# Performance work log

Measured on AMD Instinct MI355X. Metric: run time of the kernel, lower is better.

The kernel has to match this reference:

```python
import jax, jax.numpy as jnp
import numpy as np
from jax import lax

MID = 64      # mid_size -> token seq len = MID*MID = 4096
DM = 64       # d_model = in_channels
DI = 128      # d_inner = expand * d_model
DS = 16       # d_state
DC = 4        # d_conv
DTR = 4       # dt_rank = ceil(DM/16)
EPS = 1e-5


def conv3x3(x, w):
    return lax.conv_general_dilated(x, w, (1, 1), ((1, 1), (1, 1)),
                                    dimension_numbers=('NCHW', 'OIHW', 'NCHW'))


def layernorm(x, w, b):
    mu = jnp.mean(x, -1, keepdims=True)
    var = jnp.mean((x - mu) ** 2, -1, keepdims=True)
    return (x - mu) * lax.rsqrt(var + EPS) * w + b


def bilinear(x, h, w):
    b, c = x.shape[:2]
    return jax.image.resize(x, (b, c, h, w), method='bilinear', antialias=False)


def mamba(tok, in_w, conv_w, conv_b, xproj_w, dt_w, dt_b, Alog, D, out_w):
    # tok: (b, L, DM)
    b, L, _ = tok.shape
    xz = tok @ in_w.T                                # (b, L, 2*DI)
    xc, z = jnp.split(xz, 2, axis=-1)
    # causal depthwise conv1d over sequence
    xcT = xc.transpose(0, 2, 1)                      # (b, DI, L)
    xconv = lax.conv_general_dilated(xcT, conv_w, (1,), ((DC - 1, 0),),
                                     dimension_numbers=('NCH', 'OIH', 'NCH'),
                                     feature_group_count=DI)
    xconv = xconv + conv_b[None, :, None]
    u = jax.nn.silu(xconv.transpose(0, 2, 1))        # (b, L, DI)
    x_dbl = u @ xproj_w.T                            # (b, L, DTR+2*DS)
    dt, B, C = jnp.split(x_dbl, [DTR, DTR + DS], axis=-1)
    dt = jax.nn.softplus(dt @ dt_w.T + dt_b)         # (b, L, DI)
    A = -jnp.exp(Alog)                               # (DI, DS)
    dA = jnp.exp(dt[..., None] * A)                  # (b, L, DI, DS)
    dBu = dt[..., None] * B[:, :, None, :] * u[..., None]

    def step(h, xs):
        a_t, bu_t = xs
        h = a_t * h + bu_t
        return h, h

    h0 = jnp.zeros((b, DI, DS), dt.dtype)
    _, hs = lax.scan(step, h0, (dA.transpose(1, 0, 2, 3), dBu.transpose(1, 0, 2, 3)))
    y = jnp.einsum('lbns,bls->bln', hs, C) + u * D   # (b, L, DI)
    y = y * jax.nn.silu(z)
    return y @ out_w.T                               # (b, L, DM)


def setup_inputs() -> dict:
    key = jax.random.key(0)
    ks = iter(jax.random.split(key, 32))
    s = 0.02
    d = {}
    d['x'] = jax.random.normal(next(ks), (4, 64, 128, 128), jnp.float32)
    for n, shp in [('cb_w1', (64, 64, 3, 3)), ('cb_w2', (64, 64, 3, 3)),
                   ('sm_w1', (64, 64, 3, 3)), ('sm_w2', (64, 64, 3, 3))]:
        d[n] = jax.random.normal(next(ks), shp, jnp.float32) * s
    d['ln1_w'] = jnp.ones((DM,), jnp.float32); d['ln1_b'] = jnp.zeros((DM,), jnp.float32)
    d['ln2_w'] = jnp.ones((DM,), jnp.float32); d['ln2_b'] = jnp.zeros((DM,), jnp.float32)
    for p in ['m1', 'm2']:
        d[p + '_in_w'] = jax.random.normal(next(ks), (2 * DI, DM), jnp.float32) * s
        d[p + '_conv_w'] = jax.random.normal(next(ks), (DI, 1, DC), jnp.float32) * s
        d[p + '_conv_b'] = jnp.zeros((DI,), jnp.float32)
        d[p + '_xproj_w'] = jax.random.normal(next(ks), (DTR + 2 * DS, DI), jnp.float32) * s
        d[p + '_dt_w'] = jax.random.normal(next(ks), (DI, DTR), jnp.float32) * s
        d[p + '_dt_b'] = jnp.full((DI,), -2.0, jnp.float32)
        d[p + '_Alog'] = jnp.broadcast_to(jnp.log(jnp.arange(1, DS + 1, dtype=jnp.float32)), (DI, DS)).copy()
        d[p + '_D'] = jnp.ones((DI,), jnp.float32)
        d[p + '_out_w'] = jax.random.normal(next(ks), (DM, DI), jnp.float32) * s
    return d


def reference(x, cb_w1, cb_w2, ln1_w, ln1_b, ln2_w, ln2_b,
              m1_in_w, m1_conv_w, m1_conv_b, m1_xproj_w, m1_dt_w, m1_dt_b, m1_Alog, m1_D, m1_out_w,
              m2_in_w, m2_conv_w, m2_conv_b, m2_xproj_w, m2_dt_w, m2_dt_b, m2_Alog, m2_D, m2_out_w,
              sm_w1, sm_w2):
    b, c, h, w = x.shape
    xr = conv3x3(jax.nn.relu(conv3x3(x, cb_w1)), cb_w2) + x
    x_small = xr if (h, w) == (MID, MID) else bilinear(xr, MID, MID)
    tokens = x_small.reshape(b, c, MID * MID).transpose(0, 2, 1)   # (b, L, c)
    main = mamba(layernorm(tokens, ln1_w, ln1_b),
                 m1_in_w, m1_conv_w, m1_conv_b, m1_xproj_w, m1_dt_w, m1_dt_b, m1_Alog, m1_D, m1_out_w)
    gate_feat = mamba(layernorm(tokens, ln2_w, ln2_b),
                      m2_in_w, m2_conv_w, m2_conv_b, m2_xproj_w, m2_dt_w, m2_dt_b, m2_Alog, m2_D, m2_out_w)
    gate = jax.nn.softmax(gate_feat, axis=1)                       # softmax over token dim
    tokens = tokens + gate * main
    feat = tokens.transpose(0, 2, 1).reshape(b, c, MID, MID)
    if (h, w) != (MID, MID):
        feat = bilinear(feat, h, w)
    return conv3x3(jax.nn.relu(conv3x3(feat, sm_w1)), sm_w2)
```

## Files before the change

### kernel.cpp

```cpp
#include <hip/hip_runtime.h>

typedef unsigned int u32;
typedef unsigned short u16;
typedef __attribute__((ext_vector_type(8))) short short8;
typedef __attribute__((ext_vector_type(4))) float f32x4;

__device__ __forceinline__ float sigmoidf_(float x){
  return 1.f / (1.f + __expf(-x));
}
__device__ __forceinline__ u16 f2bf(float f){
  union { float f; u32 i; } v; v.f = f;
  u32 r = v.i + 0x7fffu + ((v.i >> 16) & 1u);
  return (u16)(r >> 16);
}
__device__ __forceinline__ float bf2f(u32 u){
  union { float f; u32 i; } v; v.i = (u & 0xffffu) << 16; return v.f;
}

__global__ void k_wswz2b(const float* __restrict__ wA, u16* __restrict__ WHA, u16* __restrict__ WLA,
                         const float* __restrict__ wB, u16* __restrict__ WHB, u16* __restrict__ WLB,
                         u16* __restrict__ BPH, u16* __restrict__ BPL){
  int gidx = blockIdx.x * 256 + threadIdx.x;
  if (gidx < 73728){
    int sel = gidx >= 36864;
    int idx = gidx - sel * 36864;
    const float* w = sel ? wB : wA;
    u16* WH = sel ? WHB : WHA;
    u16* WL = sel ? WLB : WLA;
    int j    = idx & 7;
    int lane = (idx >> 3) & 63;
    int nt   = (idx >> 9) & 3;
    int kc   = (idx >> 11) & 1;
    int t    = idx >> 12;
    int ic = kc * 32 + ((lane >> 4) & 3) * 8 + j;
    int oc = nt * 16 + (lane & 15);
    float v = w[(oc * 64 + ic) * 9 + t];
    u16 h = f2bf(v);
    u16 l = f2bf(v - bf2f(h));
    WH[idx] = h; WL[idx] = l;
  } else {
    int i = gidx - 73728;
    if (i >= 2064) return;
    int b = i / 516, p = i - b * 516;
    int y, x;
    if (p < 130){ y = 0; x = p; }
    else if (p < 260){ y = 129; x = p - 130; }
    else if (p < 388){ y = p - 260 + 1; x = 0; }
    else { y = p - 388 + 1; x = 129; }
    size_t o = (((size_t)b * 130 + y) * 130 + x) * 64;
    uint4 z = make_uint4(0, 0, 0, 0);
#pragma unroll
    for (int q = 0; q < 8; q++){
      *(uint4*)(BPH + o + q * 8) = z;
      *(uint4*)(BPL + o + q * 8) = z;
    }
  }
}

__global__ __launch_bounds__(256) void k_prep(const float* __restrict__ src,
                                              u16* __restrict__ PH, u16* __restrict__ PL){
  __shared__ float ld[64 * 129];
  int yp = blockIdx.x;
  int b  = blockIdx.y;
  int ys = yp - 1;
  int tid = threadIdx.x;
  if ((u32)ys < 128u){
    for (int i = tid; i < 8192; i += 256){
      int c = i >> 7, x = i & 127;
      ld[c * 129 + x] = src[((size_t)(b * 64 + c) * 128 + ys) * 128 + x];
    }
  }
  __syncthreads();
  for (int i = tid; i < 130 * 64; i += 256){
    int xp = i >> 6, c = i & 63;
    float v = 0.f;
    if ((u32)ys < 128u && (u32)(xp - 1) < 128u) v = ld[c * 129 + (xp - 1)];
    u16 h = f2bf(v);
    u16 l = f2bf(v - bf2f(h));
    size_t o = (((size_t)b * 130 + yp) * 130 + xp) * 64 + c;
    PH[o] = h; PL[o] = l;
  }
}

__global__ __launch_bounds__(256) void k_prepup(const float* __restrict__ FEAT,
                                                u16* __restrict__ PH, u16* __restrict__ PL){
  __shared__ float ld0[64 * 65], ld1[64 * 65];
  int yp = blockIdx.x;
  int b  = blockIdx.y;
  int ys = yp - 1;
  int tid = threadIdx.x;
  float wy = 0.f;
  if ((u32)ys < 128u){
    float ay = 0.5f * ys - 0.25f;
    int fy = (int)floorf(ay); wy = ay - fy;
    int y0s = fy < 0 ? 0 : fy, y1s = fy + 1 > 63 ? 63 : fy + 1;
    for (int i = tid; i < 1024; i += 256){
      int c = i >> 4, x4 = (i & 15) * 4;
      float4 a0 = *(const float4*)&FEAT[((size_t)(b * 64 + c) * 64 + y0s) * 64 + x4];
      float4 a1 = *(const float4*)&FEAT[((size_t)(b * 64 + c) * 64 + y1s) * 64 + x4];
      ld0[c * 65 + x4 + 0] = a0.x; ld0[c * 65 + x4 + 1] = a0.y;
      ld0[c * 65 + x4 + 2] = a0.z; ld0[c * 65 + x4 + 3] = a0.w;
      ld1[c * 65 + x4 + 0] = a1.x; ld1[c * 65 + x4 + 1] = a1.y;
      ld1[c * 65 + x4 + 2] = a1.z; ld1[c * 65 + x4 + 3] = a1.w;
    }
  }
  __syncthreads();
  for (int i = tid; i < 130 * 64; i += 256){
    int xp = i >> 6, c = i & 63;
    float v = 0.f;
    int xs = xp - 1;
    if ((u32)ys < 128u && (u32)xs < 128u){
      float ax = 0.5f * xs - 0.25f;
      int fx = (int)floorf(ax); float wx = ax - fx;
      int x0s = fx < 0 ? 0 : fx, x1s = fx + 1 > 63 ? 63 : fx + 1;
      float v0 = (1.f - wx) * ld0[c * 65 + x0s] + wx * ld0[c * 65 + x1s];
      float v1 = (1.f - wx) * ld1[c * 65 + x0s] + wx * ld1[c * 65 + x1s];
      v = (1.f - wy) * v0 + wy * v1;
    }
    u16 h = f2bf(v);
    u16 l = f2bf(v - bf2f(h));
    size_t o = (((size_t)b * 130 + yp) * 130 + xp) * 64 + c;
    PH[o] = h; PL[o] = l;
  }
}

__global__ __launch_bounds__(256) void k_convm(
    const u16* __restrict__ PH, const u16* __restrict__ PL,
    const u16* __restrict__ WH, const u16* __restrict__ WL,
    const float* __restrict__ resid,
    u16* __restrict__ OBH, u16* __restrict__ OBL,
    float* __restrict__ OUTF, float* __restrict__ T, float* __restrict__ NT,
    int mode)
{
  __shared__ __align__(16) u32 smem[9024];
  u16* Ah_s = (u16*)smem;
  u16* Al_s = Ah_s + 5760;
  int tid = threadIdx.x;
  int lane = tid & 63, w = tid >> 6;
  int quad = lane >> 4, lcol = lane & 15;
  int b = blockIdx.z, y0 = blockIdx.y * 8, x0 = blockIdx.x * 16;

  f32x4 acc[2][4];
#pragma unroll
  for (int mt = 0; mt < 2; mt++)
#pragma unroll
    for (int nt = 0; nt < 4; nt++)
      acc[mt][nt] = (f32x4){0.f, 0.f, 0.f, 0.f};

  for (int kc = 0; kc < 2; kc++){
    __syncthreads();
    for (int i = tid; i < 720; i += 256){
      int q = i & 3;
      int rc = i >> 2;
      int r = rc / 18, c = rc - r * 18;
      size_t so = (((size_t)b * 130 + y0 + r) * 130 + (x0 + c)) * 64 + kc * 32 + q * 8;
      int de = (r * 18 + c) * 32 + q * 8;
      *(uint4*)(Ah_s + de) = *(const uint4*)(PH + so);
      *(uint4*)(Al_s + de) = *(const uint4*)(PL + so);
    }
    __syncthreads();
#pragma unroll
    for (int t = 0; t < 9; t++){
      int dy = t / 3, dx = t - dy * 3;
      short8 bh[4], bl[4];
#pragma unroll
      for (int nt = 0; nt < 4; nt++){
        int o = ((t * 2 + kc) * 4 + nt) * 512 + lane * 8;
        bh[nt] = *(const short8*)(WH + o);
        bl[nt] = *(const short8*)(WL + o);
      }
      short8 ah[2], al[2];
#pragma unroll
      for (int mt = 0; mt < 2; mt++){
        int e = ((w * 2 + mt + dy) * 18 + (lcol + dx)) * 32 + quad * 8;
        ah[mt] = *(const short8*)(Ah_s + e);
        al[mt] = *(const short8*)(Al_s + e);
      }
#pragma unroll
      for (int mt = 0; mt < 2; mt++)
#pragma unroll
        for (int nt = 0; nt < 4; nt++){
          acc[mt][nt] = __builtin_amdgcn_mfma_f32_16x16x32_bf16(ah[mt], bh[nt], acc[mt][nt], 0, 0, 0);
          acc[mt][nt] = __builtin_amdgcn_mfma_f32_16x16x32_bf16(ah[mt], bl[nt], acc[mt][nt], 0, 0, 0);
          acc[mt][nt] = __builtin_amdgcn_mfma_f32_16x16x32_bf16(al[mt], bh[nt], acc[mt][nt], 0, 0, 0);
        }
    }
  }

  __syncthreads();
  if (mode == 0){
    u32* epi = smem;
#pragma unroll
    for (int mt = 0; mt < 2; mt++){
      int row = w * 2 + mt;
#pragma unroll
      for (int nt = 0; nt < 4; nt++){
#pragma unroll
        for (int reg = 0; reg < 4; reg++){
          float v = fmaxf(acc[mt][nt][reg], 0.f);
          u32 h = f2bf(v);
          u32 l = f2bf(v - bf2f(h));
          int ccol = quad * 4 + reg;
          int oc = nt * 16 + lcol;
          epi[(row * 16 + ccol) * 66 + oc] = h | (l << 16);
        }
      }
    }
    __syncthreads();
    for (int i = tid; i < 8192; i += 256){
      int px = i >> 6, oc = i & 63;
      int row = px >> 4, ccol = px & 15;
      u32 pk = epi[px * 66 + oc];
      size_t o = (((size_t)b * 130 + y0 + row + 1) * 130 + (x0 + ccol + 1)) * 64 + oc;
      OBH[o] = (u16)pk;
      OBL[o] = (u16)(pk >> 16);
    }
  } else {
    float* epi = (float*)smem;
#pragma unroll
    for (int mt = 0; mt < 2; mt++){
      int row = w * 2 + mt;
#pragma unroll
      for (int nt = 0; nt < 4; nt++){
#pragma unroll
        for (int reg = 0; reg < 4; reg++){
          int px = row * 16 + quad * 4 + reg;
          int oc = nt * 16 + lcol;
          epi[oc * 131 + px] = acc[mt][nt][reg];
        }
      }
    }
    __syncthreads();
    if (mode == 1){
      for (int i = tid; i < 8192; i += 256){
        int oc = i >> 7, px = i & 127;
        int row = px >> 4, c = px & 15;
        size_t o = (((size_t)b * 64 + oc) * 128 + y0 + row) * 128 + x0 + c;
        float v = epi[oc * 131 + px];
        if (resid) v += resid[o];
        OUTF[o] = v;
      }
    } else {
      for (int i = tid; i < 8192; i += 256){
        int oc = i >> 7, px = i & 127;
        int row = px >> 4, c = px & 15;
        size_t o = (((size_t)b * 64 + oc) * 128 + y0 + row) * 128 + x0 + c;
        epi[oc * 131 + px] += resid[o];
      }
      __syncthreads();
      float* redS  = (float*)smem + 8384;
      float* redQ  = redS + 288;
      float* stats = redQ + 288;
      int token = tid & 31, cgrp = tid >> 5;
      int tr = token >> 3, tc = token & 7;
      float av[8]; float s = 0.f, q = 0.f;
      int p0 = (2 * tr) * 16 + 2 * tc;
#pragma unroll
      for (int j = 0; j < 8; j++){
        int c = cgrp * 8 + j;
        const float* ep = epi + c * 131;
        float v = 0.25f * (ep[p0] + ep[p0 + 1] + ep[p0 + 16] + ep[p0 + 17]);
        av[j] = v; s += v; q = fmaf(v, v, q);
      }
      redS[token * 9 + cgrp] = s;
      redQ[token * 9 + cgrp] = q;
      __syncthreads();
      if (tid < 32){
        float S = 0.f, Q = 0.f;
        for (int g = 0; g < 8; g++){ S += redS[tid * 9 + g]; Q += redQ[tid * 9 + g]; }
        float mu = S * (1.f / 64.f);
        float var = Q * (1.f / 64.f) - mu * mu;
        stats[tid * 2] = mu;
        stats[tid * 2 + 1] = rsqrtf(var + 1e-5f);
      }
      __syncthreads();
      float mu = stats[token * 2], inv = stats[token * 2 + 1];
      int l = (blockIdx.y * 4 + tr) * 64 + blockIdx.x * 8 + tc;
      size_t to = ((size_t)b * 4096 + l) * 64 + cgrp * 8;
#pragma unroll
      for (int j = 0; j < 8; j++){
        T[to + j] = av[j];
        NT[to + j] = (av[j] - mu) * inv;
      }
    }
  }
}

__global__ __launch_bounds__(256) void k_fold2(
    const float* __restrict__ Wa, const float* __restrict__ lnwa, const float* __restrict__ lnba,
    float* __restrict__ W2a, float* __restrict__ B2a,
    const float* __restrict__ Wb, const float* __restrict__ lnwb, const float* __restrict__ lnbb,
    float* __restrict__ W2b, float* __restrict__ B2b){
  int m = blockIdx.x;
  const float* W   = m ? Wb   : Wa;
  const float* lnw = m ? lnwb : lnwa;
  const float* lnb = m ? lnbb : lnba;
  float* W2 = m ? W2b : W2a;
  float* B2 = m ? B2b : B2a;
  __shared__ float gw[64], gb[64];
  int j = threadIdx.x;
  if (j < 64){ gw[j] = lnw[j]; gb[j] = lnb[j]; }
  __syncthreads();
  float bias = 0.f;
#pragma unroll
  for (int k4 = 0; k4 < 16; k4++){
    float4 wv = *(const float4*)&W[j * 64 + k4 * 4];
    W2[j * 64 + k4 * 4 + 0] = wv.x * gw[k4 * 4 + 0];
    W2[j * 64 + k4 * 4 + 1] = wv.y * gw[k4 * 4 + 1];
    W2[j * 64 + k4 * 4 + 2] = wv.z * gw[k4 * 4 + 2];
    W2[j * 64 + k4 * 4 + 3] = wv.w * gw[k4 * 4 + 3];
    bias = fmaf(wv.x, gb[k4 * 4 + 0], bias);
    bias = fmaf(wv.y, gb[k4 * 4 + 1], bias);
    bias = fmaf(wv.z, gb[k4 * 4 + 2], bias);
    bias = fmaf(wv.w, gb[k4 * 4 + 3], bias);
  }
  B2[j] = bias;
}

__global__ __launch_bounds__(256) void k_inprojdw(
    const float* __restrict__ NT,
    const float* __restrict__ W2a, const float* __restrict__ B2a,
    float* __restrict__ Ua, float* __restrict__ Za,
    const float* __restrict__ cwa, const float* __restrict__ cba,
    const float* __restrict__ W2b, const float* __restrict__ B2b,
    float* __restrict__ Ub, float* __restrict__ Zb,
    const float* __restrict__ cwb, const float* __restrict__ cbb)
{
  __shared__ float wL[64 * 68];
  __shared__ float xcs[67 * 68];
  int mz = blockIdx.z;
  const float* W2 = mz ? W2b : W2a;
  const float* B2 = mz ? B2b : B2a;
  float* U = mz ? Ub : Ua;
  float* Z  = mz ? Zb : Za;
  const float* cw = mz ? cwb : cwa;
  const float* cb = mz ? cbb : cba;
  int tid = threadIdx.x;
  int t0 = blockIdx.x * 64;
  int j0 = blockIdx.y * 64;
  for (int i = tid; i < 4096; i += 256){
    int jl = i >> 6, k = i & 63;
    wL[jl * 68 + k] = W2[(size_t)(j0 + jl) * 64 + k];
  }
  __syncthreads();
  int tq = tid >> 4, cg = tid & 15;
  const float* ntp = NT + (size_t)(t0 + tq * 4) * 64;
  float acc[4][4];
#pragma unroll
  for (int c = 0; c < 4; c++){
    float bias = B2[j0 + cg + c * 16];
#pragma unroll
    for (int t = 0; t < 4; t++) acc[t][c] = bias;
  }
#pragma unroll 4
  for (int k4 = 0; k4 < 16; k4++){
    float4 lv[4];
#pragma unroll
    for (int t = 0; t < 4; t++)
      lv[t] = *(const float4*)(ntp + t * 64 + k4 * 4);
    float4 wv[4];
#pragma unroll
    for (int c = 0; c < 4; c++)
      wv[c] = *(const float4*)&wL[(cg + c * 16) * 68 + k4 * 4];
#pragma unroll
    for (int t = 0; t < 4; t++)
#pragma unroll
      for (int c = 0; c < 4; c++){
        acc[t][c] = fmaf(lv[t].x, wv[c].x, acc[t][c]);
        acc[t][c] = fmaf(lv[t].y, wv[c].y, acc[t][c]);
        acc[t][c] = fmaf(lv[t].z, wv[c].z, acc[t][c]);
        acc[t][c] = fmaf(lv[t].w, wv[c].w, acc[t][c]);
      }
  }
  if (j0 < 128){
    int isStart = ((t0 & 4095) == 0);
    if (tid < 192){
      int e = tid >> 6, col = tid & 63;
      float v = 0.f;
      if (!isStart){
        const float* np = NT + (size_t)(t0 - 3 + e) * 64;
        float a2 = B2[j0 + col];
#pragma unroll 4
        for (int k = 0; k < 64; k += 4){
          float4 nv = *(const float4*)(np + k);
          float4 wv = *(const float4*)&wL[col * 68 + k];
          a2 = fmaf(nv.x, wv.x, fmaf(nv.y, wv.y, fmaf(nv.z, wv.z, fmaf(nv.w, wv.w, a2))));
        }
        v = a2;
      }
      xcs[e * 68 + col] = v;
    }
#pragma unroll
    for (int t = 0; t < 4; t++)
#pragma unroll
      for (int c = 0; c < 4; c++)
        xcs[(3 + tq * 4 + t) * 68 + cg + c * 16] = acc[t][c];
    __syncthreads();
#pragma unroll
    for (int c = 0; c < 4; c++){
      int lc = cg + c * 16;
      int ch = j0 + lc;
      float4 wv = *(const float4*)(cw + ch * 4);
      float bias = cb[ch];
#pragma unroll
      for (int t = 0; t < 4; t++){
        int row = 3 + tq * 4 + t;
        float a = bias;
        a = fmaf(wv.w, xcs[row * 68 + lc], a);
        a = fmaf(wv.z, xcs[(row - 1) * 68 + lc], a);
        a = fmaf(wv.y, xcs[(row - 2) * 68 + lc], a);
        a = fmaf(wv.x, xcs[(row - 3) * 68 + lc], a);
        size_t tg = t0 + tq * 4 + t;
        U[tg * 128 + ch] = a * sigmoidf_(a);
      }
    }
  } else {
#pragma unroll
    for (int t = 0; t < 4; t++){
      size_t tg = t0 + tq * 4 + t;
#pragma unroll
      for (int c = 0; c < 4; c++)
        Z[tg * 128 + (j0 - 128) + cg + c * 16] = acc[t][c];
    }
  }
}

__global__ __launch_bounds__(256) void k_xprojdt(
    const float* __restrict__ U0, const float* __restrict__ XW0,
    const float* __restrict__ DTW0, const float* __restrict__ DTB0,
    float* __restrict__ DBL0, float* __restrict__ DT0,
    const float* __restrict__ U1, const float* __restrict__ XW1,
    const float* __restrict__ DTW1, const float* __restrict__ DTB1,
    float* __restrict__ DBL1, float* __restrict__ DT1)
{
  __shared__ float xw[36 * 132];
  __shared__ float sdtr[128 * 4];
  int bid = blockIdx.x;
  int m = bid >> 7, blk = bid & 127;
  const float* Up   = m ? U1   : U0;
  const float* XWp  = m ? XW1  : XW0;
  const float* DTWp = m ? DTW1 : DTW0;
  const float* DTBp = m ? DTB1 : DTB0;
  float* DBLp = m ? DBL1 : DBL0;
  float* DTp  = m ? DT1  : DT0;
  int tid = threadIdx.x;
  for (int i = tid; i < 4608; i += 256)
    xw[(i >> 7) * 132 + (i & 127)] = XWp[i];
  __syncthreads();
  int slot = tid >> 2, jq = tid & 3;
  size_t tgA = (size_t)blk * 128 + slot;
  size_t tgB = tgA + 64;
  const float4* upA = (const float4*)(Up + tgA * 128);
  const float4* upB = (const float4*)(Up + tgB * 128);
  float accA[9], accB[9];
#pragma unroll
  for (int jj = 0; jj < 9; jj++){ accA[jj] = 0.f; accB[jj] = 0.f; }
  for (int k4 = 0; k4 < 32; k4++){
    float4 uA = upA[k4];
    float4 uB = upB[k4];
#pragma unroll
    for (int jj = 0; jj < 9; jj++){
      float4 w = *(const float4*)&xw[(jq * 9 + jj) * 132 + k4 * 4];
      accA[jj] = fmaf(w.x, uA.x, fmaf(w.y, uA.y, fmaf(w.z, uA.z, fmaf(w.w, uA.w, accA[jj]))));
      accB[jj] = fmaf(w.x, uB.x, fmaf(w.y, uB.y, fmaf(w.z, uB.z, fmaf(w.w, uB.w, accB[jj]))));
    }
  }
#pragma unroll
  for (int jj = 0; jj < 9; jj++){
    DBLp[tgA * 36 + jq * 9 + jj] = accA[jj];
    DBLp[tgB * 36 + jq * 9 + jj] = accB[jj];
  }
  if (jq == 0){
#pragma unroll
    for (int jj = 0; jj < 4; jj++){
      sdtr[slot * 4 + jj] = accA[jj];
      sdtr[(slot + 64) * 4 + jj] = accB[jj];
    }
  }
  __syncthreads();
  int ch = tid & 127, half = tid >> 7;
  float4 wv = *(const float4*)(DTWp + ch * 4);
  float bias = DTBp[ch];
  for (int i = 0; i < 64; i++){
    int tl = half * 64 + i;
    float4 d = *(const float4*)&sdtr[tl * 4];
    float x = bias;
    x = fmaf(wv.x, d.x, x); x = fmaf(wv.y, d.y, x);
    x = fmaf(wv.z, d.z, x); x = fmaf(wv.w, d.w, x);
    x = fmaxf(x, 0.f) + log1pf(__expf(-fabsf(x)));
    DTp[((size_t)blk * 128 + tl) * 128 + ch] = x;
  }
}

__global__ __launch_bounds__(256) void k_scanA(
    const float* __restrict__ DT0, const float* __restrict__ DBL0, const float* __restrict__ U0,
    const float* __restrict__ AL0,
    const float* __restrict__ DT1, const float* __restrict__ DBL1, const float* __restrict__ U1,
    const float* __restrict__ AL1,
    float* __restrict__ HF, float* __restrict__ AP)
{
  __shared__ float sdt[64 * 65], su[64 * 65], sB[16 * 68];
  int bid = blockIdx.x;
  int cg = bid & 1;
  int c  = (bid >> 1) & 63;
  int b  = (bid >> 7) & 3;
  int m  = bid >> 9;
  const float* DTp  = m ? DT1  : DT0;
  const float* DBLp = m ? DBL1 : DBL0;
  const float* Up   = m ? U1   : U0;
  const float* ALp  = m ? AL1  : AL0;
  int tid = threadIdx.x;
  int lane = tid & 63, w = tid >> 6;
  int lcol = lane & 15, q = lane >> 4;
  int chL = w * 16 + lcol;
  int n = cg * 64 + chL;
  size_t base = (size_t)b * 4096 + c * 64;
  for (int i = tid; i < 4096; i += 256){
    int ch = i & 63, l = i >> 6;
    size_t off = (base + l) * 128 + cg * 64 + ch;
    sdt[l * 65 + ch] = DTp[off];
    su[l * 65 + ch]  = Up[off];
  }
  for (int i = tid; i < 1024; i += 256){
    int s = i & 15, l = i >> 4;
    sB[s * 68 + l] = DBLp[(base + l) * 36 + 4 + s];
  }
  float A1[4];
#pragma unroll
  for (int j = 0; j < 4; j++) A1[j] = -__expf(ALp[n * 16 + q * 4 + j]);
  __syncthreads();
  float h[4] = {0.f, 0.f, 0.f, 0.f};
  float ap[4] = {1.f, 1.f, 1.f, 1.f};
#pragma unroll
  for (int l4 = 0; l4 < 16; l4++){
    float4 Bv[4];
#pragma unroll
    for (int j = 0; j < 4; j++) Bv[j] = *(const float4*)&sB[(q * 4 + j) * 68 + l4 * 4];
#pragma unroll
    for (int jj = 0; jj < 4; jj++){
      int l = l4 * 4 + jj;
      float dt = sdt[l * 65 + chL];
      float u  = su[l * 65 + chL];
      float dtu = dt * u;
#pragma unroll
      for (int j = 0; j < 4; j++){
        float a = __expf(dt * A1[j]);
        h[j] = fmaf(a, h[j], dtu * (&Bv[j].x)[jj]);
        ap[j] *= a;
      }
    }
  }
  size_t o = ((size_t)((m * 4 + b) * 64 + c)) * 2048 + n * 16 + q * 4;
  *(float4*)&HF[o] = make_float4(h[0], h[1], h[2], h[3]);
  *(float4*)&AP[o] = make_float4(ap[0], ap[1], ap[2], ap[3]);
}

__global__ __launch_bounds__(64) void k_scanB(
    const float* __restrict__ HF, const float* __restrict__ AP, float* __restrict__ HIN)
{
  int r = blockIdx.x * 64 + threadIdx.x;
  int q = r >> 11;
  int p = r & 2047;
  float h = 0.f;
  for (int c = 0; c < 64; c++){
    size_t o = (size_t)(q * 64 + c) * 2048 + p;
    HIN[o] = h;
    h = fmaf(AP[o], h, HF[o]);
  }
}

__global__ __launch_bounds__(256) void k_scanC(
    const float* __restrict__ DT0, const float* __restrict__ DBL0, const float* __restrict__ U0,
    const float* __restrict__ AL0, const float* __restrict__ D0, float* __restrict__ Y0,
    const float* __restrict__ DT1, const float* __restrict__ DBL1, const float* __restrict__ U1,
    const float* __restrict__ AL1, const float* __restrict__ D1, float* __restrict__ Y1,
    const float* __restrict__ HIN)
{
  __shared__ float sdt[64 * 65], su[64 * 65], sB[16 * 68], sC[16 * 68];
  int bid = blockIdx.x;
  int cg = bid & 1;
  int c  = (bid >> 1) & 63;
  int b  = (bid >> 7) & 3;
  int m  = bid >> 9;
  const float* DTp  = m ? DT1  : DT0;
  const float* DBLp = m ? DBL1 : DBL0;
  const float* Up   = m ? U1   : U0;
  const float* ALp  = m ? AL1  : AL0;
  const float* Dp   = m ? D1   : D0;
  float*       Yp   = m ? Y1   : Y0;
  int tid = threadIdx.x;
  int lane = tid & 63, w = tid >> 6;
  int lcol = lane & 15, q = lane >> 4;
  int chL = w * 16 + lcol;
  int n = cg * 64 + chL;
  size_t base = (size_t)b * 4096 + c * 64;
  for (int i = tid; i < 4096; i += 256){
    int ch = i & 63, l = i >> 6;
    size_t off = (base + l) * 128 + cg * 64 + ch;
    sdt[l * 65 + ch] = DTp[off];
    su[l * 65 + ch]  = Up[off];
  }
  for (int i = tid; i < 1024; i += 256){
    int s = i & 15, l = i >> 4;
    size_t ob = (base + l) * 36;
    sB[s * 68 + l] = DBLp[ob + 4 + s];
    sC[s * 68 + l] = DBLp[ob + 20 + s];
  }
  float A1[4];
#pragma unroll
  for (int j = 0; j < 4; j++) A1[j] = -__expf(ALp[n * 16 + q * 4 + j]);
  float Dn = Dp[n];
  float4 hv = *(const float4*)&HIN[((size_t)((m * 4 + b) * 64 + c)) * 2048 + n * 16 + q * 4];
  float h[4] = {hv.x, hv.y, hv.z, hv.w};
  __syncthreads();
#pragma unroll
  for (int l4 = 0; l4 < 16; l4++){
    float4 Bv[4], Cv[4];
#pragma unroll
    for (int j = 0; j < 4; j++){
      Bv[j] = *(const float4*)&sB[(q * 4 + j) * 68 + l4 * 4];
      Cv[j] = *(const float4*)&sC[(q * 4 + j) * 68 + l4 * 4];
    }
#pragma unroll
    for (int jj = 0; jj < 4; jj++){
      int l = l4 * 4 + jj;
      float dt = sdt[l * 65 + chL];
      float u  = su[l * 65 + chL];
      float dtu = dt * u;
      float p = 0.f;
#pragma unroll
      for (int j = 0; j < 4; j++){
        float a = __expf(dt * A1[j]);
        h[j] = fmaf(a, h[j], dtu * (&Bv[j].x)[jj]);
        p = fmaf(h[j], (&Cv[j].x)[jj], p);
      }
      p += __shfl_xor(p, 16);
      p += __shfl_xor(p, 32);
      if (q == 0)
        Yp[(base + l) * 128 + n] = fmaf(u, Dn, p);
    }
  }
}

__global__ __launch_bounds__(256) void k_outproj(
    const float* __restrict__ Y0, const float* __restrict__ Zg0,
    const float* __restrict__ W0, float* __restrict__ OUT0,
    const float* __restrict__ Y1, const float* __restrict__ Zg1,
    const float* __restrict__ W1, float* __restrict__ OUT1)
{
  __shared__ float yl[16 * 128];
  __shared__ float wT[128 * 65];
  int m = blockIdx.y;
  const float* Y  = m ? Y1  : Y0;
  const float* Zg = m ? Zg1 : Zg0;
  const float* W  = m ? W1  : W0;
  float* OUT = m ? OUT1 : OUT0;
  int tid = threadIdx.x;
  size_t t0 = (size_t)blockIdx.x * 16;
  for (int i = tid; i < 2048; i += 256){
    float z = Zg[t0 * 128 + i];
    yl[i] = Y[t0 * 128 + i] * (z * sigmoidf_(z));
  }
  for (int i = tid; i < 8192; i += 256){
    int k = i & 127, j = i >> 7;
    wT[k * 65 + j] = W[j * 128 + k];
  }
  __syncthreads();
  int j = tid & 63;
  int tg = tid >> 6;
  float acc[4] = {0.f, 0.f, 0.f, 0.f};
  for (int k = 0; k < 128; k += 4){
    float w0 = wT[k * 65 + j], w1 = wT[(k+1) * 65 + j];
    float w2 = wT[(k+2) * 65 + j], w3 = wT[(k+3) * 65 + j];
#pragma unroll
    for (int t = 0; t < 4; t++){
      float4 yv = *(const float4*)&yl[(tg * 4 + t) * 128 + k];
      acc[t] = fmaf(w0, yv.x, fmaf(w1, yv.y, fmaf(w2, yv.z, fmaf(w3, yv.w, acc[t]))));
    }
  }
#pragma unroll
  for (int t = 0; t < 4; t++)
    OUT[(t0 + tg * 4 + t) * 64 + j] = acc[t];
}

__global__ void k_smA(const float* __restrict__ G, float* __restrict__ P){
  int bid = blockIdx.x;
  int b = bid >> 6, lc = bid & 63;
  int tid = threadIdx.x;
  int j = tid & 63, part = tid >> 6;
  size_t base = (size_t)b * 4096 + lc * 64;
  float mx = -3.4e38f;
  for (int i = 0; i < 16; i++){
    int l = part + i * 4;
    mx = fmaxf(mx, G[(base + l) * 64 + j]);
  }
  float sm = 0.f;
  for (int i = 0; i < 16; i++){
    int l = part + i * 4;
    sm += __expf(G[(base + l) * 64 + j] - mx);
  }
  __shared__ float sM[256], sS[256];
  sM[tid] = mx; sS[tid] = sm;
  __syncthreads();
  if (tid < 64){
    float M = sM[tid], S = sS[tid];
    for (int p = 1; p < 4; p++){
      float m2 = sM[p * 64 + tid], s2 = sS[p * 64 + tid];
      float Mn = fmaxf(M, m2);
      S = S * __expf(M - Mn) + s2 * __expf(m2 - Mn);
      M = Mn;
    }
    P[(bid * 64 + tid) * 2] = M;
    P[(bid * 64 + tid) * 2 + 1] = S;
  }
}

__global__ void k_smB(const float* __restrict__ P, float* __restrict__ F){
  int tid = threadIdx.x;
  int b = tid >> 6, j = tid & 63;
  float M = -3.4e38f, S = 0.f;
  for (int lc = 0; lc < 64; lc++){
    int idx = ((b * 64 + lc) * 64 + j) * 2;
    float m2 = P[idx], s2 = P[idx + 1];
    float Mn = fmaxf(M, m2);
    S = S * __expf(M - Mn) + s2 * __expf(m2 - Mn);
    M = Mn;
  }
  F[(b * 64 + j) * 2] = M;
  F[(b * 64 + j) * 2 + 1] = S;
}

__global__ void k_combine(const float* __restrict__ T, const float* __restrict__ MAIN,
                          const float* __restrict__ G, const float* __restrict__ F,
                          float* __restrict__ FEAT){
  int bid = blockIdx.x;
  int b = bid >> 6, row = bid & 63;
  int tid = threadIdx.x;
  int j = tid & 63, ls = tid >> 6;
  __shared__ float tile[64 * 65];
  float M = F[(b * 64 + j) * 2], invS = 1.f / F[(b * 64 + j) * 2 + 1];
  size_t lbase = (size_t)b * 4096 + row * 64;
  for (int i = 0; i < 16; i++){
    int col = ls + i * 4;
    size_t off = (lbase + col) * 64 + j;
    float g = __expf(G[off] - M) * invS;
    tile[col * 65 + j] = T[off] + g * MAIN[off];
  }
  __syncthreads();
  int colw = tid & 63, jr = tid >> 6;
  for (int jj = jr; jj < 64; jj += 4)
    FEAT[(((size_t)b * 64 + jj) * 64 + row) * 64 + colw] = tile[colw * 65 + jj];
}

extern "C" void kernel_launch(void* const* d_in, const int* in_sizes, int n_in,
                              void* d_out, int out_size, void* d_ws, size_t ws_size,
                              hipStream_t stream) {
  const size_t P1A = 0, P1B = 4326400;
  const size_t MB0 = 0, MB1 = 10027008;
  const size_t O_LN = 0, O_XC = 1048576, O_Z = 3145728, O_U = 5242880,
               O_DT = 7340032, O_DBL = 9437184;
  const size_t TOK = 20054016, OUT0 = 21102592, OUT1 = 22151168;
  const size_t FEAT = 23208448;
  const size_t P3A = 4194304, P3B = 8520704;
  const size_t WA_H = 19000000, WA_L = 19018432, WB_H = 19036864, WB_L = 19055296;
  const size_t PADN = 2163200;
  const size_t SMP = 0, SMF = 65536;
  const size_t W2_0 = 21102592, B2_0 = 21118976, W2_1 = 21119232, B2_1 = 21135616;
  const size_t TOTAL = 24257024;
  if (ws_size < TOTAL * 4) return;

  float* ws = (float*)d_ws;
  const float* X   = (const float*)d_in[0];
  const float* CB1 = (const float*)d_in[1];
  const float* CB2 = (const float*)d_in[2];
  const float* SW1 = (const float*)d_in[3];
  const float* SW2 = (const float*)d_in[4];
  const float* LNW[2] = { (const float*)d_in[5], (const float*)d_in[7] };
  const float* LNB[2] = { (const float*)d_in[6], (const float*)d_in[8] };
  const float *INW[2], *CW[2], *CBb[2], *XPW[2], *DTW[2], *DTB[2], *AL[2], *DD[2], *OW[2];
  for (int m = 0; m < 2; m++){
    int p = 9 + m * 9;
    INW[m] = (const float*)d_in[p + 0];
    CW[m]  = (const float*)d_in[p + 1];
    CBb[m] = (const float*)d_in[p + 2];
    XPW[m] = (const float*)d_in[p + 3];
    DTW[m] = (const float*)d_in[p + 4];
    DTB[m] = (const float*)d_in[p + 5];
    AL[m]  = (const float*)d_in[p + 6];
    DD[m]  = (const float*)d_in[p + 7];
    OW[m]  = (const float*)d_in[p + 8];
  }

  u16* wah = (u16*)(ws + WA_H); u16* wal = (u16*)(ws + WA_L);
  u16* wbh = (u16*)(ws + WB_H); u16* wbl = (u16*)(ws + WB_L);

  {
    u16* pah = (u16*)(ws + P1A); u16* pal = pah + PADN * 2;
    u16* pbh = (u16*)(ws + P1B); u16* pbl = pbh + PADN * 2;
    k_wswz2b<<<297, 256, 0, stream>>>(CB1, wah, wal, CB2, wbh, wbl, pbh, pbl);
    k_prep<<<dim3(130, 4), 256, 0, stream>>>(X, pah, pal);
    k_convm<<<dim3(8, 16, 4), 256, 0, stream>>>(pah, pal, wah, wal, nullptr,
                                                pbh, pbl, nullptr, nullptr, nullptr, 0);
    k_convm<<<dim3(8, 16, 4), 256, 0, stream>>>(pbh, pbl, wbh, wbl, X,
                                                nullptr, nullptr, nullptr,
                                                ws + TOK, ws + MB0 + O_LN, 2);
  }

  k_fold2<<<2, 256, 0, stream>>>(INW[0], LNW[0], LNB[0], ws + W2_0, ws + B2_0,
                                 INW[1], LNW[1], LNB[1], ws + W2_1, ws + B2_1);
  k_inprojdw<<<dim3(256, 4, 2), 256, 0, stream>>>(
      ws + MB0 + O_LN,
      ws + W2_0, ws + B2_0, ws + MB0 + O_U, ws + MB0 + O_Z, CW[0], CBb[0],
      ws + W2_1, ws + B2_1, ws + MB1 + O_U, ws + MB1 + O_Z, CW[1], CBb[1]);
  k_xprojdt<<<256, 256, 0, stream>>>(
      ws + MB0 + O_U, XPW[0], DTW[0], DTB[0], ws + MB0 + O_DBL, ws + MB0 + O_DT,
      ws + MB1 + O_U, XPW[1], DTW[1], DTB[1], ws + MB1 + O_DBL, ws + MB1 + O_DT);

  float* HF  = ws + MB0 + O_XC;
  float* AP  = ws + MB0 + O_XC + 1048576;
  float* HIN = ws + MB0 + O_LN;

  k_scanA<<<1024, 256, 0, stream>>>(
      ws + MB0 + O_DT, ws + MB0 + O_DBL, ws + MB0 + O_U, AL[0],
      ws + MB1 + O_DT, ws + MB1 + O_DBL, ws + MB1 + O_U, AL[1],
      HF, AP);
  k_scanB<<<256, 64, 0, stream>>>(HF, AP, HIN);
  k_scanC<<<1024, 256, 0, stream>>>(
      ws + MB0 + O_DT, ws + MB0 + O_DBL, ws + MB0 + O_U, AL[0], DD[0], ws + MB0 + O_XC,
      ws + MB1 + O_DT, ws + MB1 + O_DBL, ws + MB1 + O_U, AL[1], DD[1], ws + MB1 + O_XC,
      HIN);

  k_outproj<<<dim3(1024, 2), 256, 0, stream>>>(
      ws + MB0 + O_XC, ws + MB0 + O_Z, OW[0], ws + OUT0,
      ws + MB1 + O_XC, ws + MB1 + O_Z, OW[1], ws + OUT1);

  k_smA<<<256, 256, 0, stream>>>(ws + OUT1, ws + SMP);
  k_smB<<<1, 256, 0, stream>>>(ws + SMP, ws + SMF);
  k_combine<<<256, 256, 0, stream>>>(ws + TOK, ws + OUT0, ws + OUT1, ws + SMF, ws + FEAT);

  {
    u16* pah = (u16*)(ws + P3A); u16* pal = pah + PADN * 2;
    u16* pbh = (u16*)(ws + P3B); u16* pbl = pbh + PADN * 2;
    k_wswz2b<<<297, 256, 0, stream>>>(SW1, wah, wal, SW2, wbh, wbl, pbh, pbl);
    k_prepup<<<dim3(130, 4), 256, 0, stream>>>(ws + FEAT, pah, pal);
    k_convm<<<dim3(8, 16, 4), 256, 0, stream>>>(pah, pal, wah, wal, nullptr,
                                                pbh, pbl, nullptr, nullptr, nullptr, 0);
    k_convm<<<dim3(8, 16, 4), 256, 0, stream>>>(pbh, pbl, wbh, wbl, nullptr,
                                                nullptr, nullptr, (float*)d_out,
                                                nullptr, nullptr, 1);
  }
}
```

Before: 393.6 us.

## Enlarge conv tiles, recompute dt inside scan kernels, batch scanB loads

The conv kernel tile grows from 8x16 to 16x16 pixels per block, with 4 M-tiles per wave. This halves the grid and raises shared memory use, trading occupancy for more weight reuse and less halo overhead. The dt projection and softplus move out of k_xprojdt into both scan kernels, removing the large DT tensor's write and two reads at the cost of recomputing it twice. scanB now loads 8 steps of AP/HF before its serial recurrence to expose memory-level parallelism.

```diff
diff --git a/kernel.cpp b/kernel.cpp
--- a/kernel.cpp
+++ b/kernel.cpp
@@ -132,29 +132,29 @@
     float* __restrict__ OUTF, float* __restrict__ T, float* __restrict__ NT,
     int mode)
 {
-  __shared__ __align__(16) u32 smem[9024];
+  __shared__ __align__(16) u32 smem[17344];
   u16* Ah_s = (u16*)smem;
-  u16* Al_s = Ah_s + 5760;
+  u16* Al_s = Ah_s + 10368;
   int tid = threadIdx.x;
   int lane = tid & 63, w = tid >> 6;
   int quad = lane >> 4, lcol = lane & 15;
-  int b = blockIdx.z, y0 = blockIdx.y * 8, x0 = blockIdx.x * 16;
-
-  f32x4 acc[2][4];
-#pragma unroll
-  for (int mt = 0; mt < 2; mt++)
+  int b = blockIdx.z, y0 = blockIdx.y * 16, x0 = blockIdx.x * 16;
+
+  f32x4 acc[4][4];
+#pragma unroll
+  for (int mt = 0; mt < 4; mt++)
 #pragma unroll
     for (int nt = 0; nt < 4; nt++)
       acc[mt][nt] = (f32x4){0.f, 0.f, 0.f, 0.f};
 
   for (int kc = 0; kc < 2; kc++){
     __syncthreads();
-    for (int i = tid; i < 720; i += 256){
+    for (int i = tid; i < 1296; i += 256){
       int q = i & 3;
       int rc = i >> 2;
       int r = rc / 18, c = rc - r * 18;
       size_t so = (((size_t)b * 130 + y0 + r) * 130 + (x0 + c)) * 64 + kc * 32 + q * 8;
-      int de = (r * 18 + c) * 32 + q * 8;
+      int de = rc * 32 + q * 8;
       *(uint4*)(Ah_s + de) = *(const uint4*)(PH + so);
       *(uint4*)(Al_s + de) = *(const uint4*)(PL + so);
     }
@@ -169,15 +169,15 @@
         bh[nt] = *(const short8*)(WH + o);
         bl[nt] = *(const short8*)(WL + o);
       }
-      short8 ah[2], al[2];
-#pragma unroll
-      for (int mt = 0; mt < 2; mt++){
-        int e = ((w * 2 + mt + dy) * 18 + (lcol + dx)) * 32 + quad * 8;
+      short8 ah[4], al[4];
+#pragma unroll
+      for (int mt = 0; mt < 4; mt++){
+        int e = ((w * 4 + mt + dy) * 18 + (lcol + dx)) * 32 + quad * 8;
         ah[mt] = *(const short8*)(Ah_s + e);
         al[mt] = *(const short8*)(Al_s + e);
       }
 #pragma unroll
-      for (int mt = 0; mt < 2; mt++)
+      for (int mt = 0; mt < 4; mt++)
 #pragma unroll
         for (int nt = 0; nt < 4; nt++){
           acc[mt][nt] = __builtin_amdgcn_mfma_f32_16x16x32_bf16(ah[mt], bh[nt], acc[mt][nt], 0, 0, 0);
@@ -191,8 +191,8 @@
   if (mode == 0){
     u32* epi = smem;
 #pragma unroll
-    for (int mt = 0; mt < 2; mt++){
-      int row = w * 2 + mt;
+    for (int mt = 0; mt < 4; mt++){
+      int row = w * 4 + mt;
 #pragma unroll
       for (int nt = 0; nt < 4; nt++){
 #pragma unroll
@@ -207,7 +207,7 @@
       }
     }
     __syncthreads();
-    for (int i = tid; i < 8192; i += 256){
+    for (int i = tid; i < 16384; i += 256){
       int px = i >> 6, oc = i & 63;
       int row = px >> 4, ccol = px & 15;
       u32 pk = epi[px * 66 + oc];
@@ -218,56 +218,56 @@
   } else {
     float* epi = (float*)smem;
 #pragma unroll
-    for (int mt = 0; mt < 2; mt++){
-      int row = w * 2 + mt;
+    for (int mt = 0; mt < 4; mt++){
+      int row = w * 4 + mt;
 #pragma unroll
       for (int nt = 0; nt < 4; nt++){
 #pragma unroll
         for (int reg = 0; reg < 4; reg++){
           int px = row * 16 + quad * 4 + reg;
           int oc = nt * 16 + lcol;
-          epi[oc * 131 + px] = acc[mt][nt][reg];
+          epi[oc * 259 + px] = acc[mt][nt][reg];
         }
       }
     }
     __syncthreads();
     if (mode == 1){
-      for (int i = tid; i < 8192; i += 256){
-        int oc = i >> 7, px = i & 127;
+      for (int i = tid; i < 16384; i += 256){
+        int oc = i >> 8, px = i & 255;
         int row = px >> 4, c = px & 15;
         size_t o = (((size_t)b * 64 + oc) * 128 + y0 + row) * 128 + x0 + c;
-        float v = epi[oc * 131 + px];
+        float v = epi[oc * 259 + px];
         if (resid) v += resid[o];
         OUTF[o] = v;
       }
     } else {
-      for (int i = tid; i < 8192; i += 256){
-        int oc = i >> 7, px = i & 127;
+      for (int i = tid; i < 16384; i += 256){
+        int oc = i >> 8, px = i & 255;
         int row = px >> 4, c = px & 15;
         size_t o = (((size_t)b * 64 + oc) * 128 + y0 + row) * 128 + x0 + c;
-        epi[oc * 131 + px] += resid[o];
+        epi[oc * 259 + px] += resid[o];
       }
       __syncthreads();
-      float* redS  = (float*)smem + 8384;
-      float* redQ  = redS + 288;
-      float* stats = redQ + 288;
-      int token = tid & 31, cgrp = tid >> 5;
+      float* redS  = (float*)smem + 16576;
+      float* redQ  = redS + 320;
+      float* stats = redQ + 320;
+      int token = tid & 63, cg2 = tid >> 6;
       int tr = token >> 3, tc = token & 7;
-      float av[8]; float s = 0.f, q = 0.f;
+      float av[16]; float s = 0.f, q = 0.f;
       int p0 = (2 * tr) * 16 + 2 * tc;
 #pragma unroll
-      for (int j = 0; j < 8; j++){
-        int c = cgrp * 8 + j;
-        const float* ep = epi + c * 131;
+      for (int j = 0; j < 16; j++){
+        int c = cg2 * 16 + ((j + tr) & 15);
+        const float* ep = epi + c * 259;
         float v = 0.25f * (ep[p0] + ep[p0 + 1] + ep[p0 + 16] + ep[p0 + 17]);
         av[j] = v; s += v; q = fmaf(v, v, q);
       }
-      redS[token * 9 + cgrp] = s;
-      redQ[token * 9 + cgrp] = q;
+      redS[token * 5 + cg2] = s;
+      redQ[token * 5 + cg2] = q;
       __syncthreads();
-      if (tid < 32){
+      if (tid < 64){
         float S = 0.f, Q = 0.f;
-        for (int g = 0; g < 8; g++){ S += redS[tid * 9 + g]; Q += redQ[tid * 9 + g]; }
+        for (int g = 0; g < 4; g++){ S += redS[tid * 5 + g]; Q += redQ[tid * 5 + g]; }
         float mu = S * (1.f / 64.f);
         float var = Q * (1.f / 64.f) - mu * mu;
         stats[tid * 2] = mu;
@@ -275,12 +275,13 @@
       }
       __syncthreads();
       float mu = stats[token * 2], inv = stats[token * 2 + 1];
-      int l = (blockIdx.y * 4 + tr) * 64 + blockIdx.x * 8 + tc;
-      size_t to = ((size_t)b * 4096 + l) * 64 + cgrp * 8;
-#pragma unroll
-      for (int j = 0; j < 8; j++){
-        T[to + j] = av[j];
-        NT[to + j] = (av[j] - mu) * inv;
+      int l = (blockIdx.y * 8 + tr) * 64 + blockIdx.x * 8 + tc;
+      size_t to = ((size_t)b * 4096 + l) * 64;
+#pragma unroll
+      for (int j = 0; j < 16; j++){
+        int c = cg2 * 16 + ((j + tr) & 15);
+        T[to + c] = av[j];
+        NT[to + c] = (av[j] - mu) * inv;
       }
     }
   }
@@ -426,23 +427,15 @@
 }
 
 __global__ __launch_bounds__(256) void k_xprojdt(
-    const float* __restrict__ U0, const float* __restrict__ XW0,
-    const float* __restrict__ DTW0, const float* __restrict__ DTB0,
-    float* __restrict__ DBL0, float* __restrict__ DT0,
-    const float* __restrict__ U1, const float* __restrict__ XW1,
-    const float* __restrict__ DTW1, const float* __restrict__ DTB1,
-    float* __restrict__ DBL1, float* __restrict__ DT1)
+    const float* __restrict__ U0, const float* __restrict__ XW0, float* __restrict__ DBL0,
+    const float* __restrict__ U1, const float* __restrict__ XW1, float* __restrict__ DBL1)
 {
   __shared__ float xw[36 * 132];
-  __shared__ float sdtr[128 * 4];
   int bid = blockIdx.x;
   int m = bid >> 7, blk = bid & 127;
   const float* Up   = m ? U1   : U0;
   const float* XWp  = m ? XW1  : XW0;
-  const float* DTWp = m ? DTW1 : DTW0;
-  const float* DTBp = m ? DTB1 : DTB0;
   float* DBLp = m ? DBL1 : DBL0;
-  float* DTp  = m ? DT1  : DT0;
   int tid = threadIdx.x;
   for (int i = tid; i < 4608; i += 256)
     xw[(i >> 7) * 132 + (i & 127)] = XWp[i];
@@ -470,45 +463,26 @@
     DBLp[tgA * 36 + jq * 9 + jj] = accA[jj];
     DBLp[tgB * 36 + jq * 9 + jj] = accB[jj];
   }
-  if (jq == 0){
-#pragma unroll
-    for (int jj = 0; jj < 4; jj++){
-      sdtr[slot * 4 + jj] = accA[jj];
-      sdtr[(slot + 64) * 4 + jj] = accB[jj];
-    }
-  }
-  __syncthreads();
-  int ch = tid & 127, half = tid >> 7;
-  float4 wv = *(const float4*)(DTWp + ch * 4);
-  float bias = DTBp[ch];
-  for (int i = 0; i < 64; i++){
-    int tl = half * 64 + i;
-    float4 d = *(const float4*)&sdtr[tl * 4];
-    float x = bias;
-    x = fmaf(wv.x, d.x, x); x = fmaf(wv.y, d.y, x);
-    x = fmaf(wv.z, d.z, x); x = fmaf(wv.w, d.w, x);
-    x = fmaxf(x, 0.f) + log1pf(__expf(-fabsf(x)));
-    DTp[((size_t)blk * 128 + tl) * 128 + ch] = x;
-  }
 }
 
 __global__ __launch_bounds__(256) void k_scanA(
-    const float* __restrict__ DT0, const float* __restrict__ DBL0, const float* __restrict__ U0,
-    const float* __restrict__ AL0,
-    const float* __restrict__ DT1, const float* __restrict__ DBL1, const float* __restrict__ U1,
-    const float* __restrict__ AL1,
+    const float* __restrict__ DBL0, const float* __restrict__ U0, const float* __restrict__ AL0,
+    const float* __restrict__ DTW0, const float* __restrict__ DTB0,
+    const float* __restrict__ DBL1, const float* __restrict__ U1, const float* __restrict__ AL1,
+    const float* __restrict__ DTW1, const float* __restrict__ DTB1,
     float* __restrict__ HF, float* __restrict__ AP)
 {
-  __shared__ float sdt[64 * 65], su[64 * 65], sB[16 * 68];
+  __shared__ float sdt[64 * 65], su[64 * 65], sB[16 * 68], sdtr[256];
   int bid = blockIdx.x;
   int cg = bid & 1;
   int c  = (bid >> 1) & 63;
   int b  = (bid >> 7) & 3;
   int m  = bid >> 9;
-  const float* DTp  = m ? DT1  : DT0;
   const float* DBLp = m ? DBL1 : DBL0;
   const float* Up   = m ? U1   : U0;
   const float* ALp  = m ? AL1  : AL0;
+  const float* DTWp = m ? DTW1 : DTW0;
+  const float* DTBp = m ? DTB1 : DTB0;
   int tid = threadIdx.x;
   int lane = tid & 63, w = tid >> 6;
   int lcol = lane & 15, q = lane >> 4;
@@ -517,13 +491,31 @@
   size_t base = (size_t)b * 4096 + c * 64;
   for (int i = tid; i < 4096; i += 256){
     int ch = i & 63, l = i >> 6;
-    size_t off = (base + l) * 128 + cg * 64 + ch;
-    sdt[l * 65 + ch] = DTp[off];
-    su[l * 65 + ch]  = Up[off];
+    su[l * 65 + ch] = Up[(base + l) * 128 + cg * 64 + ch];
   }
   for (int i = tid; i < 1024; i += 256){
     int s = i & 15, l = i >> 4;
     sB[s * 68 + l] = DBLp[(base + l) * 36 + 4 + s];
+  }
+  if (tid < 256){
+    int l = tid >> 2, jj = tid & 3;
+    sdtr[tid] = DBLp[(base + l) * 36 + jj];
+  }
+  __syncthreads();
+  {
+    int chF = tid & 63;
+    float4 wdt = *(const float4*)(DTWp + (cg * 64 + chF) * 4);
+    float bdt = DTBp[cg * 64 + chF];
+#pragma unroll
+    for (int k = 0; k < 16; k++){
+      int l = (tid >> 6) + k * 4;
+      float4 d = *(const float4*)&sdtr[l * 4];
+      float x = bdt;
+      x = fmaf(wdt.x, d.x, x); x = fmaf(wdt.y, d.y, x);
+      x = fmaf(wdt.z, d.z, x); x = fmaf(wdt.w, d.w, x);
+      x = fmaxf(x, 0.f) + log1pf(__expf(-fabsf(x)));
+      sdt[l * 65 + chF] = x;
+    }
   }
   float A1[4];
 #pragma unroll
@@ -561,31 +553,44 @@
   int r = blockIdx.x * 64 + threadIdx.x;
   int q = r >> 11;
   int p = r & 2047;
+  size_t base = (size_t)q * 64 * 2048 + p;
   float h = 0.f;
-  for (int c = 0; c < 64; c++){
-    size_t o = (size_t)(q * 64 + c) * 2048 + p;
-    HIN[o] = h;
-    h = fmaf(AP[o], h, HF[o]);
+  for (int c8 = 0; c8 < 8; c8++){
+    float a[8], f[8];
+#pragma unroll
+    for (int j = 0; j < 8; j++){
+      size_t o = base + (size_t)(c8 * 8 + j) * 2048;
+      a[j] = AP[o]; f[j] = HF[o];
+    }
+#pragma unroll
+    for (int j = 0; j < 8; j++){
+      size_t o = base + (size_t)(c8 * 8 + j) * 2048;
+      HIN[o] = h;
+      h = fmaf(a[j], h, f[j]);
+    }
   }
 }
 
 __global__ __launch_bounds__(256) void k_scanC(
-    const float* __restrict__ DT0, const float* __restrict__ DBL0, const float* __restrict__ U0,
-    const float* __restrict__ AL0, const float* __restrict__ D0, float* __restrict__ Y0,
-    const float* __restrict__ DT1, const float* __restrict__ DBL1, const float* __restrict__ U1,
-    const float* __restrict__ AL1, const float* __restrict__ D1, float* __restrict__ Y1,
+    const float* __restrict__ DBL0, const float* __restrict__ U0, const float* __restrict__ AL0,
+    const float* __restrict__ DTW0, const float* __restrict__ DTB0,
+    const float* __restrict__ D0, float* __restrict__ Y0,
+    const float* __restrict__ DBL1, const float* __restrict__ U1, const float* __restrict__ AL1,
+    const float* __restrict__ DTW1, const float* __restrict__ DTB1,
+    const float* __restrict__ D1, float* __restrict__ Y1,
     const float* __restrict__ HIN)
 {
-  __shared__ float sdt[64 * 65], su[64 * 65], sB[16 * 68], sC[16 * 68];
+  __shared__ float sdt[64 * 65], su[64 * 65], sB[16 * 68], sC[16 * 68], sdtr[256];
   int bid = blockIdx.x;
   int cg = bid & 1;
   int c  = (bid >> 1) & 63;
   int b  = (bid >> 7) & 3;
   int m  = bid >> 9;
-  const float* DTp  = m ? DT1  : DT0;
   const float* DBLp = m ? DBL1 : DBL0;
   const float* Up   = m ? U1   : U0;
   const float* ALp  = m ? AL1  : AL0;
+  const float* DTWp = m ? DTW1 : DTW0;
+  const float* DTBp = m ? DTB1 : DTB0;
   const float* Dp   = m ? D1   : D0;
   float*       Yp   = m ? Y1   : Y0;
   int tid = threadIdx.x;
@@ -596,15 +601,33 @@
   size_t base = (size_t)b * 4096 + c * 64;
   for (int i = tid; i < 4096; i += 256){
     int ch = i & 63, l = i >> 6;
-    size_t off = (base + l) * 128 + cg * 64 + ch;
-    sdt[l * 65 + ch] = DTp[off];
-    su[l * 65 + ch]  = Up[off];
+    su[l * 65 + ch] = Up[(base + l) * 128 + cg * 64 + ch];
   }
   for (int i = tid; i < 1024; i += 256){
     int s = i & 15, l = i >> 4;
     size_t ob = (base + l) * 36;
     sB[s * 68 + l] = DBLp[ob + 4 + s];
     sC[s * 68 + l] = DBLp[ob + 20 + s];
+  }
+  if (tid < 256){
+    int l = tid >> 2, jj = tid & 3;
+    sdtr[tid] = DBLp[(base + l) * 36 + jj];
+  }
+  __syncthreads();
+  {
+    int chF = tid & 63;
+    float4 wdt = *(const float4*)(DTWp + (cg * 64 + chF) * 4);
+    float bdt = DTBp[cg * 64 + chF];
+#pragma unroll
+    for (int k = 0; k < 16; k++){
+      int l = (tid >> 6) + k * 4;
+      float4 d = *(const float4*)&sdtr[l * 4];
+      float x = bdt;
+      x = fmaf(wdt.x, d.x, x); x = fmaf(wdt.y, d.y, x);
+      x = fmaf(wdt.z, d.z, x); x = fmaf(wdt.w, d.w, x);
+      x = fmaxf(x, 0.f) + log1pf(__expf(-fabsf(x)));
+      sdt[l * 65 + chF] = x;
+    }
   }
   float A1[4];
 #pragma unroll
@@ -758,7 +781,7 @@
   const size_t P1A = 0, P1B = 4326400;
   const size_t MB0 = 0, MB1 = 10027008;
   const size_t O_LN = 0, O_XC = 1048576, O_Z = 3145728, O_U = 5242880,
-               O_DT = 7340032, O_DBL = 9437184;
+               O_DBL = 9437184;
   const size_t TOK = 20054016, OUT0 = 21102592, OUT1 = 22151168;
   const size_t FEAT = 23208448;
   const size_t P3A = 4194304, P3B = 8520704;
@@ -799,11 +822,11 @@
     u16* pbh = (u16*)(ws + P1B); u16* pbl = pbh + PADN * 2;
     k_wswz2b<<<297, 256, 0, stream>>>(CB1, wah, wal, CB2, wbh, wbl, pbh, pbl);
     k_prep<<<dim3(130, 4), 256, 0, stream>>>(X, pah, pal);
-    k_convm<<<dim3(8, 16, 4), 256, 0, stream>>>(pah, pal, wah, wal, nullptr,
-                                                pbh, pbl, nullptr, nullptr, nullptr, 0);
-    k_convm<<<dim3(8, 16, 4), 256, 0, stream>>>(pbh, pbl, wbh, wbl, X,
-                                                nullptr, nullptr, nullptr,
-                                                ws + TOK, ws + MB0 + O_LN, 2);
+    k_convm<<<dim3(8, 8, 4), 256, 0, stream>>>(pah, pal, wah, wal, nullptr,
+                                               pbh, pbl, nullptr, nullptr, nullptr, 0);
+    k_convm<<<dim3(8, 8, 4), 256, 0, stream>>>(pbh, pbl, wbh, wbl, X,
+                                               nullptr, nullptr, nullptr,
+                                               ws + TOK, ws + MB0 + O_LN, 2);
   }
 
   k_fold2<<<2, 256, 0, stream>>>(INW[0], LNW[0], LNB[0], ws + W2_0, ws + B2_0,
@@ -813,21 +836,21 @@
       ws + W2_0, ws + B2_0, ws + MB0 + O_U, ws + MB0 + O_Z, CW[0], CBb[0],
       ws + W2_1, ws + B2_1, ws + MB1 + O_U, ws + MB1 + O_Z, CW[1], CBb[1]);
   k_xprojdt<<<256, 256, 0, stream>>>(
-      ws + MB0 + O_U, XPW[0], DTW[0], DTB[0], ws + MB0 + O_DBL, ws + MB0 + O_DT,
-      ws + MB1 + O_U, XPW[1], DTW[1], DTB[1], ws + MB1 + O_DBL, ws + MB1 + O_DT);
+      ws + MB0 + O_U, XPW[0], ws + MB0 + O_DBL,
+      ws + MB1 + O_U, XPW[1], ws + MB1 + O_DBL);
 
   float* HF  = ws + MB0 + O_XC;
   float* AP  = ws + MB0 + O_XC + 1048576;
   float* HIN = ws + MB0 + O_LN;
 
   k_scanA<<<1024, 256, 0, stream>>>(
-      ws + MB0 + O_DT, ws + MB0 + O_DBL, ws + MB0 + O_U, AL[0],
-      ws + MB1 + O_DT, ws + MB1 + O_DBL, ws + MB1 + O_U, AL[1],
+      ws + MB0 + O_DBL, ws + MB0 + O_U, AL[0], DTW[0], DTB[0],
+      ws + MB1 + O_DBL, ws + MB1 + O_U, AL[1], DTW[1], DTB[1],
       HF, AP);
   k_scanB<<<256, 64, 0, stream>>>(HF, AP, HIN);
   k_scanC<<<1024, 256, 0, stream>>>(
-      ws + MB0 + O_DT, ws + MB0 + O_DBL, ws + MB0 + O_U, AL[0], DD[0], ws + MB0 + O_XC,
-      ws + MB1 + O_DT, ws + MB1 + O_DBL, ws + MB1 + O_U, AL[1], DD[1], ws + MB1 + O_XC,
+      ws + MB0 + O_DBL, ws + MB0 + O_U, AL[0], DTW[0], DTB[0], DD[0], ws + MB0 + O_XC,
+      ws + MB1 + O_DBL, ws + MB1 + O_U, AL[1], DTW[1], DTB[1], DD[1], ws + MB1 + O_XC,
       HIN);
 
   k_outproj<<<dim3(1024, 2), 256, 0, stream>>>(
@@ -843,10 +866,10 @@
     u16* pbh = (u16*)(ws + P3B); u16* pbl = pbh + PADN * 2;
     k_wswz2b<<<297, 256, 0, stream>>>(SW1, wah, wal, SW2, wbh, wbl, pbh, pbl);
     k_prepup<<<dim3(130, 4), 256, 0, stream>>>(ws + FEAT, pah, pal);
-    k_convm<<<dim3(8, 16, 4), 256, 0, stream>>>(pah, pal, wah, wal, nullptr,
-                                                pbh, pbl, nullptr, nullptr, nullptr, 0);
-    k_convm<<<dim3(8, 16, 4), 256, 0, stream>>>(pbh, pbl, wbh, wbl, nullptr,
-                                                nullptr, nullptr, (float*)d_out,
-                                                nullptr, nullptr, 1);
-  }
-}
+    k_convm<<<dim3(8, 8, 4), 256, 0, stream>>>(pah, pal, wah, wal, nullptr,
+                                               pbh, pbl, nullptr, nullptr, nullptr, 0);
+    k_convm<<<dim3(8, 8, 4), 256, 0, stream>>>(pbh, pbl, wbh, wbl, nullptr,
+                                               nullptr, nullptr, (float*)d_out,
+                                               nullptr, nullptr, 1);
+  }
+}
```

New measurement: 395.5 us. About the same (+0.5%).
